# Performance work log

Hardware: AMD Instinct MI355X
Metric: run time of the kernel (lower is better)

Reference implementation:

```python
import jax, jax.numpy as jnp
import numpy as np

N_NODES = 100000
N_EDGES = 2000000
N_GRAPHS = 2000
IN_DIM = 7
EDGE_DIM = 4
HID = 32
N_CLASSES = 2
NEG_SLOPE = 0.2
BN_EPS = 1e-5


def setup_inputs() -> dict:
    key = jax.random.key(0)
    ks = jax.random.split(key, 16)
    x = jax.random.normal(ks[0], (N_NODES, IN_DIM), dtype=jnp.float32)
    edge_index = jax.random.randint(ks[1], (2, N_EDGES), 0, N_NODES, dtype=jnp.int64)
    batch = jnp.sort(jax.random.randint(ks[2], (N_NODES,), 0, N_GRAPHS, dtype=jnp.int64))
    edge_attr = jax.random.normal(ks[3], (N_EDGES, EDGE_DIM), dtype=jnp.float32)
    s = 0.1
    W0 = jax.random.normal(ks[4], (IN_DIM, HID), dtype=jnp.float32) * s
    W12 = jax.random.normal(ks[5], (2, HID, HID), dtype=jnp.float32) * s
    att_src = jax.random.normal(ks[6], (3, HID), dtype=jnp.float32) * s
    att_dst = jax.random.normal(ks[7], (3, HID), dtype=jnp.float32) * s
    lin_edge = jax.random.normal(ks[8], (3, EDGE_DIM, HID), dtype=jnp.float32) * s
    att_edge = jax.random.normal(ks[9], (3, HID), dtype=jnp.float32) * s
    bias = jnp.zeros((3, HID), dtype=jnp.float32)
    bn_gamma = jnp.ones((3, HID), dtype=jnp.float32)
    bn_beta = jnp.zeros((3, HID), dtype=jnp.float32)
    fc_W = jax.random.normal(ks[10], (HID, N_CLASSES), dtype=jnp.float32) * s
    fc_b = jnp.zeros((N_CLASSES,), dtype=jnp.float32)
    return dict(x=x, edge_index=edge_index, batch=batch, edge_attr=edge_attr,
                W0=W0, W12=W12, att_src=att_src, att_dst=att_dst,
                lin_edge=lin_edge, att_edge=att_edge, bias=bias,
                bn_gamma=bn_gamma, bn_beta=bn_beta, fc_W=fc_W, fc_b=fc_b)


def gat_layer(x, src, dst, edge_attr, W, a_src, a_dst, We, a_edge, b):
    # PyG GATConv, heads=1, add_self_loops=False: edge_attr conditions attention only.
    N = x.shape[0]
    h = x @ W                                   # [N, H]
    e = edge_attr @ We                          # [E, H]
    score = ((h * a_src).sum(-1)[src]
             + (h * a_dst).sum(-1)[dst]
             + (e * a_edge).sum(-1))            # [E]
    score = jax.nn.leaky_relu(score, NEG_SLOPE)
    m = jax.ops.segment_max(score, dst, num_segments=N)
    w = jnp.exp(score - m[dst])
    denom = jax.ops.segment_sum(w, dst, num_segments=N)
    alpha = w / (denom[dst] + 1e-16)            # segment softmax over incoming edges
    out = jax.ops.segment_sum(h[src] * alpha[:, None], dst, num_segments=N)
    return out + b


def batchnorm(x, gamma, beta):
    mu = x.mean(axis=0)
    var = ((x - mu) ** 2).mean(axis=0)          # biased var, as torch BN normalization
    return (x - mu) * jax.lax.rsqrt(var + BN_EPS) * gamma + beta


def reference(x, edge_index, batch, edge_attr, W0, W12, att_src, att_dst,
              lin_edge, att_edge, bias, bn_gamma, bn_beta, fc_W, fc_b):
    src, dst = edge_index[0], edge_index[1]
    Ws = [W0, W12[0], W12[1]]
    h = x
    for l in range(3):
        h = gat_layer(h, src, dst, edge_attr, Ws[l], att_src[l], att_dst[l],
                      lin_edge[l], att_edge[l], bias[l])
        h = batchnorm(h, bn_gamma[l], bn_beta[l])
        h = jax.nn.relu(h)
    node_embs = h
    graph_emb = jax.ops.segment_sum(node_embs, batch, num_segments=N_GRAPHS)
    out = graph_emb @ fc_W + fc_b
    return (out, node_embs, graph_emb)
```

## Files before the change

### kernel.cpp

```cpp
#include <hip/hip_runtime.h>
#include <hip/hip_bf16.h>
#include <math.h>

#define N_NODES   100000
#define N_EDGES   2000000
#define N_GRAPHS  2000
#define IN_DIM    7
#define EDGE_DIM  4
#define HID       32
#define N_CLASSES 2
#define NEG_SLOPE 0.2f
#define BN_EPS    1e-5f
#define SCAN_B    1024

__device__ __forceinline__ unsigned bfbits(float f) {
    unsigned u = __float_as_uint(f);
    return (u + 0x7FFFu + ((u >> 16) & 1u)) >> 16;
}

__global__ void k_ce_all(const float* __restrict__ lin_edge, const float* __restrict__ att_edge,
                         float* __restrict__ ce3, float* __restrict__ gsum3,
                         float* __restrict__ gsq3) {
    int t = threadIdx.x;
    if (t < 12) {
        int l = t >> 2, d = t & 3;
        float s = 0.f;
        for (int k = 0; k < HID; ++k)
            s += lin_edge[(size_t)l * EDGE_DIM * HID + d * HID + k] * att_edge[l * HID + k];
        ce3[t] = s;
    }
    if (t < 3 * HID) { gsum3[t] = 0.f; gsq3[t] = 0.f; }
}

__global__ void k_hist(const int* __restrict__ dst, int* __restrict__ deg) {
    int e = blockIdx.x * blockDim.x + threadIdx.x;
    if (e < N_EDGES) atomicAdd(deg + dst[e], 1);
}

__global__ void k_scan1(const int* __restrict__ deg, int* __restrict__ offs,
                        int* __restrict__ bsum) {
    __shared__ int wsum[16];
    int t = threadIdx.x, lane = t & 63, w = t >> 6;
    int i = blockIdx.x * SCAN_B + t;
    int v = (i < N_NODES) ? deg[i] : 0;
    int x = v;
#pragma unroll
    for (int o = 1; o < 64; o <<= 1) { int y = __shfl_up(x, o, 64); if (lane >= o) x += y; }
    if (lane == 63) wsum[w] = x;
    __syncthreads();
    if (t < 16) {
        int s = wsum[t];
#pragma unroll
        for (int o = 1; o < 16; o <<= 1) { int y = __shfl_up(s, o, 16); if (t >= o) s += y; }
        wsum[t] = s;
    }
    __syncthreads();
    int excl = (w ? wsum[w - 1] : 0) + x - v;
    if (i < N_NODES) offs[i] = excl;
    if (t == 0) bsum[blockIdx.x] = wsum[15];
}

__global__ void k_scan2(int* __restrict__ bsum, int nb) {
    __shared__ int w0;
    int t = threadIdx.x, lane = t & 63, w = t >> 6;
    int v = (t < nb) ? bsum[t] : 0;
    int x = v;
#pragma unroll
    for (int o = 1; o < 64; o <<= 1) { int y = __shfl_up(x, o, 64); if (lane >= o) x += y; }
    if (w == 0 && lane == 63) w0 = x;
    __syncthreads();
    int excl = x - v + (w ? w0 : 0);
    if (t < nb) bsum[t] = excl;
}

__global__ void k_scan3(int* __restrict__ offs, const int* __restrict__ bsum,
                        int* __restrict__ cursor) {
    int i = blockIdx.x * SCAN_B + threadIdx.x;
    if (i < N_NODES) {
        int o = offs[i] + bsum[blockIdx.x];
        offs[i] = o;
        cursor[i] = o;
    }
}

__global__ void k_scatter(const int* __restrict__ src, const int* __restrict__ dst,
                          const float4* __restrict__ eattr, const float* __restrict__ ce3,
                          int* __restrict__ cursor, int4* __restrict__ pack) {
    int e = blockIdx.x * blockDim.x + threadIdx.x;
    if (e >= N_EDGES) return;
    float4 ea = eattr[e];
    float e0 = ea.x * ce3[0] + ea.y * ce3[1] + ea.z * ce3[2] + ea.w * ce3[3];
    float e1 = ea.x * ce3[4] + ea.y * ce3[5] + ea.z * ce3[6] + ea.w * ce3[7];
    float e2 = ea.x * ce3[8] + ea.y * ce3[9] + ea.z * ce3[10] + ea.w * ce3[11];
    int d = dst[e];
    int pos = atomicAdd(cursor + d, 1);
    pack[pos] = make_int4(src[e], d,
                          (int)(bfbits(e0) | (bfbits(e1) << 16)),
                          (int)bfbits(e2));
}

template <int INDIM, bool BN>
__global__ void k_linear(const float* __restrict__ in, const float* __restrict__ W,
                         const float* __restrict__ a_src, const float* __restrict__ a_dst,
                         const float* __restrict__ gsum, const float* __restrict__ gsq,
                         const float* __restrict__ gamma, const float* __restrict__ beta,
                         __hip_bfloat16* __restrict__ h, float* __restrict__ asrc,
                         float* __restrict__ adst) {
    __shared__ float Ws[INDIM * HID];
    for (int i = threadIdx.x; i < INDIM * HID; i += blockDim.x) Ws[i] = W[i];
    __syncthreads();
    int g = threadIdx.x >> 5, k = threadIdx.x & 31;
    int n = blockIdx.x * 8 + g;
    if (n >= N_NODES) return;
    float xv;
    if (BN) {
        const float invN = 1.f / (float)N_NODES;
        float mu = gsum[k] * invN;
        float var = gsq[k] * invN - mu * mu;
        var = fmaxf(var, 0.f);
        float scl = rsqrtf(var + BN_EPS) * gamma[k];
        float v = (in[(size_t)n * INDIM + k] - mu) * scl + beta[k];
        xv = fmaxf(v, 0.f);
    } else {
        xv = (k < INDIM) ? in[(size_t)n * INDIM + k] : 0.f;
    }
    float acc = 0.f;
#pragma unroll
    for (int d = 0; d < INDIM; ++d) acc += __shfl(xv, d, 32) * Ws[d * HID + k];
    h[(size_t)n * HID + k] = __float2bfloat16(acc);
    float vs = acc * a_src[k];
    float vd = acc * a_dst[k];
#pragma unroll
    for (int m = 16; m > 0; m >>= 1) {
        vs += __shfl_xor(vs, m, 32);
        vd += __shfl_xor(vd, m, 32);
    }
    if (k == 0) { asrc[n] = vs; adst[n] = vd; }
}

template <int L>
__global__ void k_edgew(const int4* __restrict__ pack, const float* __restrict__ asrc,
                        const float* __restrict__ adst, int2* __restrict__ rec) {
    int e = blockIdx.x * blockDim.x + threadIdx.x;
    if (e >= N_EDGES) return;
    int4 pk = pack[e];
    unsigned z = (unsigned)pk.z;
    float edot;
    if (L == 0)      edot = __uint_as_float((z & 0xFFFFu) << 16);
    else if (L == 1) edot = __uint_as_float(z & 0xFFFF0000u);
    else             edot = __uint_as_float(((unsigned)pk.w & 0xFFFFu) << 16);
    float sc = asrc[pk.x] + adst[pk.y] + edot;
    sc = fmaxf(sc, NEG_SLOPE * sc);
    float w = __expf(sc);
    rec[e] = make_int2(pk.x, __float_as_int(w));
}

__global__ void k_aggr(const int2* __restrict__ rec, const int* __restrict__ offs,
                       const int* __restrict__ endp, const __hip_bfloat16* __restrict__ hb,
                       const float* __restrict__ bias, float* __restrict__ out,
                       float* __restrict__ gsum, float* __restrict__ gsq) {
    __shared__ float ssum[HID], ssq[HID];
    if (threadIdx.x < HID) { ssum[threadIdx.x] = 0.f; ssq[threadIdx.x] = 0.f; }
    __syncthreads();
    int g = threadIdx.x >> 5;
    int lane = threadIdx.x & 31;
    int sub = lane >> 4;
    int c2 = lane & 15;
    int n = blockIdx.x * 8 + g;
    if (n < N_NODES) {
        int pbeg = offs[n], en = endp[n];
        float den = 0.f, a0 = 0.f, a1 = 0.f;
        for (int p = pbeg; p < en; p += 16) {
            int2 rc[8];
            unsigned hw[8];
#pragma unroll
            for (int m = 0; m < 8; ++m) {
                int q = p + 2 * m + sub;
                q = q < en ? q : en - 1;
                rc[m] = rec[q];
            }
#pragma unroll
            for (int m = 0; m < 8; ++m)
                hw[m] = *(const unsigned*)(hb + (size_t)rc[m].x * HID + 2 * c2);
#pragma unroll
            for (int m = 0; m < 8; ++m) {
                float w = (p + 2 * m + sub < en) ? __int_as_float(rc[m].y) : 0.f;
                den += w;
                float lo = __uint_as_float((hw[m] & 0xFFFFu) << 16);
                float hi = __uint_as_float(hw[m] & 0xFFFF0000u);
                a0 = fmaf(w, lo, a0);
                a1 = fmaf(w, hi, a1);
            }
        }
        den += __shfl_xor(den, 16, 32);
        a0  += __shfl_xor(a0, 16, 32);
        a1  += __shfl_xor(a1, 16, 32);
        if (sub == 0) {
            float inv = 1.f / (den + 1e-16f);
            float v0 = a0 * inv + bias[2 * c2];
            float v1 = a1 * inv + bias[2 * c2 + 1];
            *(float2*)(out + (size_t)n * HID + 2 * c2) = make_float2(v0, v1);
            atomicAdd(&ssum[2 * c2], v0);
            atomicAdd(&ssum[2 * c2 + 1], v1);
            atomicAdd(&ssq[2 * c2], v0 * v0);
            atomicAdd(&ssq[2 * c2 + 1], v1 * v1);
        }
    }
    __syncthreads();
    if (threadIdx.x < HID) {
        atomicAdd(gsum + threadIdx.x, ssum[threadIdx.x]);
        atomicAdd(gsq + threadIdx.x, ssq[threadIdx.x]);
    }
}

__global__ void k_bn_relu_pool(const float* __restrict__ acc, const float* __restrict__ gsum,
                               const float* __restrict__ gsq, const float* __restrict__ gamma,
                               const float* __restrict__ beta, const int* __restrict__ batch,
                               float* __restrict__ nemb, float* __restrict__ gemb) {
    int g = threadIdx.x >> 5, k = threadIdx.x & 31;
    int n = blockIdx.x * 8 + g;
    if (n >= N_NODES) return;
    const float invN = 1.f / (float)N_NODES;
    float mu = gsum[k] * invN;
    float var = gsq[k] * invN - mu * mu;
    var = fmaxf(var, 0.f);
    float scl = rsqrtf(var + BN_EPS) * gamma[k];
    float v = (acc[(size_t)n * HID + k] - mu) * scl + beta[k];
    v = fmaxf(v, 0.f);
    nemb[(size_t)n * HID + k] = v;
    atomicAdd(gemb + (size_t)batch[n] * HID + k, v);
}

__global__ void k_fc(const float* __restrict__ gemb, const float* __restrict__ W,
                     const float* __restrict__ b, float* __restrict__ out) {
    int g = blockIdx.x * blockDim.x + threadIdx.x;
    if (g >= N_GRAPHS) return;
    float a0 = b[0], a1 = b[1];
    for (int k = 0; k < HID; ++k) {
        float v = gemb[(size_t)g * HID + k];
        a0 += v * W[k * 2 + 0];
        a1 += v * W[k * 2 + 1];
    }
    out[g * 2 + 0] = a0;
    out[g * 2 + 1] = a1;
}

extern "C" void kernel_launch(void* const* d_in, const int* in_sizes, int n_in,
                              void* d_out, int out_size, void* d_ws, size_t ws_size,
                              hipStream_t stream) {
    const float* x        = (const float*)d_in[0];
    const int*   ei       = (const int*)d_in[1];
    const int*   batch    = (const int*)d_in[2];
    const float* eattr    = (const float*)d_in[3];
    const float* W0       = (const float*)d_in[4];
    const float* W12      = (const float*)d_in[5];
    const float* att_src  = (const float*)d_in[6];
    const float* att_dst  = (const float*)d_in[7];
    const float* lin_edge = (const float*)d_in[8];
    const float* att_edge = (const float*)d_in[9];
    const float* bias     = (const float*)d_in[10];
    const float* bn_gamma = (const float*)d_in[11];
    const float* bn_beta  = (const float*)d_in[12];
    const float* fc_W     = (const float*)d_in[13];
    const float* fc_b     = (const float*)d_in[14];

    const int* srcA = ei;
    const int* dstA = ei + N_EDGES;

    float* out       = (float*)d_out;
    float* node_embs = out + N_GRAPHS * N_CLASSES;
    float* graph_emb = node_embs + (size_t)N_NODES * HID;

    char* ws = (char*)d_ws;
    size_t off = 0;
    auto alloc = [&](size_t bytes) { char* p = ws + off; off += (bytes + 255) & ~(size_t)255; return p; };
    __hip_bfloat16* hT = (__hip_bfloat16*)alloc((size_t)N_NODES * HID * 2);
    float* A     = (float*)alloc((size_t)N_NODES * HID * 4);
    int4*  pack  = (int4*)alloc((size_t)N_EDGES * 16);
    int2*  rec   = (int2*)alloc((size_t)N_EDGES * 8);
    int*   deg   = (int*)alloc((size_t)N_NODES * 4);
    int*   offs  = (int*)alloc((size_t)N_NODES * 4);
    int*   cursor= (int*)alloc((size_t)N_NODES * 4);
    int*   bsum  = (int*)alloc(128 * 4);
    float* asrc  = (float*)alloc((size_t)N_NODES * 4);
    float* adst  = (float*)alloc((size_t)N_NODES * 4);
    float* ce3   = (float*)alloc(12 * 4);
    float* gsum3 = (float*)alloc(3 * HID * 4);
    float* gsq3  = (float*)alloc(3 * HID * 4);
    (void)ws_size;

    const int nodeBlocks8 = (N_NODES + 7) / 8;
    const int edgeBlocks  = (N_EDGES + 255) / 256;
    const int scanBlocks  = (N_NODES + SCAN_B - 1) / SCAN_B;

    hipMemsetAsync(deg, 0, (size_t)N_NODES * 4, stream);
    k_ce_all<<<1, 128, 0, stream>>>(lin_edge, att_edge, ce3, gsum3, gsq3);
    k_hist<<<edgeBlocks, 256, 0, stream>>>(dstA, deg);
    k_scan1<<<scanBlocks, SCAN_B, 0, stream>>>(deg, offs, bsum);
    k_scan2<<<1, 128, 0, stream>>>(bsum, scanBlocks);
    k_scan3<<<scanBlocks, SCAN_B, 0, stream>>>(offs, bsum, cursor);
    k_scatter<<<edgeBlocks, 256, 0, stream>>>(srcA, dstA, (const float4*)eattr, ce3, cursor, pack);

    k_linear<IN_DIM, false><<<nodeBlocks8, 256, 0, stream>>>(
        x, W0, att_src, att_dst, nullptr, nullptr, nullptr, nullptr, hT, asrc, adst);
    k_edgew<0><<<edgeBlocks, 256, 0, stream>>>(pack, asrc, adst, rec);
    k_aggr<<<nodeBlocks8, 256, 0, stream>>>(rec, offs, cursor, hT, bias, A, gsum3, gsq3);
    k_linear<HID, true><<<nodeBlocks8, 256, 0, stream>>>(
        A, W12, att_src + HID, att_dst + HID, gsum3, gsq3, bn_gamma, bn_beta, hT, asrc, adst);
    k_edgew<1><<<edgeBlocks, 256, 0, stream>>>(pack, asrc, adst, rec);
    k_aggr<<<nodeBlocks8, 256, 0, stream>>>(rec, offs, cursor, hT, bias + HID, A,
                                            gsum3 + HID, gsq3 + HID);
    k_linear<HID, true><<<nodeBlocks8, 256, 0, stream>>>(
        A, W12 + HID * HID, att_src + 2 * HID, att_dst + 2 * HID,
        gsum3 + HID, gsq3 + HID, bn_gamma + HID, bn_beta + HID, hT, asrc, adst);
    k_edgew<2><<<edgeBlocks, 256, 0, stream>>>(pack, asrc, adst, rec);
    k_aggr<<<nodeBlocks8, 256, 0, stream>>>(rec, offs, cursor, hT, bias + 2 * HID, A,
                                            gsum3 + 2 * HID, gsq3 + 2 * HID);

    hipMemsetAsync(graph_emb, 0, (size_t)N_GRAPHS * HID * 4, stream);
    k_bn_relu_pool<<<nodeBlocks8, 256, 0, stream>>>(A, gsum3 + 2 * HID, gsq3 + 2 * HID,
                                                    bn_gamma + 2 * HID, bn_beta + 2 * HID,
                                                    batch, node_embs, graph_emb);
    k_fc<<<(N_GRAPHS + 255) / 256, 256, 0, stream>>>(graph_emb, fc_W, fc_b, out);
}
```

Baseline: 963.4 us.

## Fuse edge-weight computation into CSR aggregation kernel

Removes the separate per-layer edge-weight kernel that read the 16-byte packed edge record, gathered asrc/adst, and wrote an 8-byte (src, weight) record. The aggregation kernel now reads the packed record directly, gathers asrc per edge, uses the node's own adst once, and computes leaky-relu and exp inline. This drops three kernel launches and the write and reread of the intermediate record array. The cost is that aggregation reads 16 bytes per edge instead of 8 and does redundant exp/gather work across the 16 lanes sharing each edge.

```diff
diff --git a/kernel.cpp b/kernel.cpp
--- a/kernel.cpp
+++ b/kernel.cpp
@@ -94,9 +94,9 @@
     float e2 = ea.x * ce3[8] + ea.y * ce3[9] + ea.z * ce3[10] + ea.w * ce3[11];
     int d = dst[e];
     int pos = atomicAdd(cursor + d, 1);
-    pack[pos] = make_int4(src[e], d,
+    pack[pos] = make_int4(src[e],
                           (int)(bfbits(e0) | (bfbits(e1) << 16)),
-                          (int)bfbits(e2));
+                          (int)bfbits(e2), 0);
 }
 
 template <int INDIM, bool BN>
@@ -139,24 +139,9 @@
 }
 
 template <int L>
-__global__ void k_edgew(const int4* __restrict__ pack, const float* __restrict__ asrc,
-                        const float* __restrict__ adst, int2* __restrict__ rec) {
-    int e = blockIdx.x * blockDim.x + threadIdx.x;
-    if (e >= N_EDGES) return;
-    int4 pk = pack[e];
-    unsigned z = (unsigned)pk.z;
-    float edot;
-    if (L == 0)      edot = __uint_as_float((z & 0xFFFFu) << 16);
-    else if (L == 1) edot = __uint_as_float(z & 0xFFFF0000u);
-    else             edot = __uint_as_float(((unsigned)pk.w & 0xFFFFu) << 16);
-    float sc = asrc[pk.x] + adst[pk.y] + edot;
-    sc = fmaxf(sc, NEG_SLOPE * sc);
-    float w = __expf(sc);
-    rec[e] = make_int2(pk.x, __float_as_int(w));
-}
-
-__global__ void k_aggr(const int2* __restrict__ rec, const int* __restrict__ offs,
+__global__ void k_aggr(const int4* __restrict__ pack, const int* __restrict__ offs,
                        const int* __restrict__ endp, const __hip_bfloat16* __restrict__ hb,
+                       const float* __restrict__ asrc, const float* __restrict__ adst,
                        const float* __restrict__ bias, float* __restrict__ out,
                        float* __restrict__ gsum, float* __restrict__ gsq) {
     __shared__ float ssum[HID], ssq[HID];
@@ -169,22 +154,33 @@
     int n = blockIdx.x * 8 + g;
     if (n < N_NODES) {
         int pbeg = offs[n], en = endp[n];
+        float ad = adst[n];
         float den = 0.f, a0 = 0.f, a1 = 0.f;
         for (int p = pbeg; p < en; p += 16) {
-            int2 rc[8];
+            int4 pk[8];
+            float as[8];
             unsigned hw[8];
 #pragma unroll
             for (int m = 0; m < 8; ++m) {
                 int q = p + 2 * m + sub;
                 q = q < en ? q : en - 1;
-                rc[m] = rec[q];
+                pk[m] = pack[q];
             }
 #pragma unroll
+            for (int m = 0; m < 8; ++m) as[m] = asrc[pk[m].x];
+#pragma unroll
             for (int m = 0; m < 8; ++m)
-                hw[m] = *(const unsigned*)(hb + (size_t)rc[m].x * HID + 2 * c2);
+                hw[m] = *(const unsigned*)(hb + (size_t)pk[m].x * HID + 2 * c2);
 #pragma unroll
             for (int m = 0; m < 8; ++m) {
-                float w = (p + 2 * m + sub < en) ? __int_as_float(rc[m].y) : 0.f;
+                unsigned z = (unsigned)pk[m].y;
+                float edot;
+                if (L == 0)      edot = __uint_as_float((z & 0xFFFFu) << 16);
+                else if (L == 1) edot = __uint_as_float(z & 0xFFFF0000u);
+                else             edot = __uint_as_float(((unsigned)pk[m].z & 0xFFFFu) << 16);
+                float sc = as[m] + ad + edot;
+                sc = fmaxf(sc, NEG_SLOPE * sc);
+                float w = (p + 2 * m + sub < en) ? __expf(sc) : 0.f;
                 den += w;
                 float lo = __uint_as_float((hw[m] & 0xFFFFu) << 16);
                 float hi = __uint_as_float(hw[m] & 0xFFFF0000u);
@@ -277,7 +273,6 @@
     __hip_bfloat16* hT = (__hip_bfloat16*)alloc((size_t)N_NODES * HID * 2);
     float* A     = (float*)alloc((size_t)N_NODES * HID * 4);
     int4*  pack  = (int4*)alloc((size_t)N_EDGES * 16);
-    int2*  rec   = (int2*)alloc((size_t)N_EDGES * 8);
     int*   deg   = (int*)alloc((size_t)N_NODES * 4);
     int*   offs  = (int*)alloc((size_t)N_NODES * 4);
     int*   cursor= (int*)alloc((size_t)N_NODES * 4);
@@ -303,19 +298,17 @@
 
     k_linear<IN_DIM, false><<<nodeBlocks8, 256, 0, stream>>>(
         x, W0, att_src, att_dst, nullptr, nullptr, nullptr, nullptr, hT, asrc, adst);
-    k_edgew<0><<<edgeBlocks, 256, 0, stream>>>(pack, asrc, adst, rec);
-    k_aggr<<<nodeBlocks8, 256, 0, stream>>>(rec, offs, cursor, hT, bias, A, gsum3, gsq3);
+    k_aggr<0><<<nodeBlocks8, 256, 0, stream>>>(pack, offs, cursor, hT, asrc, adst,
+                                               bias, A, gsum3, gsq3);
     k_linear<HID, true><<<nodeBlocks8, 256, 0, stream>>>(
         A, W12, att_src + HID, att_dst + HID, gsum3, gsq3, bn_gamma, bn_beta, hT, asrc, adst);
-    k_edgew<1><<<edgeBlocks, 256, 0, stream>>>(pack, asrc, adst, rec);
-    k_aggr<<<nodeBlocks8, 256, 0, stream>>>(rec, offs, cursor, hT, bias + HID, A,
-                                            gsum3 + HID, gsq3 + HID);
+    k_aggr<1><<<nodeBlocks8, 256, 0, stream>>>(pack, offs, cursor, hT, asrc, adst,
+                                               bias + HID, A, gsum3 + HID, gsq3 + HID);
     k_linear<HID, true><<<nodeBlocks8, 256, 0, stream>>>(
         A, W12 + HID * HID, att_src + 2 * HID, att_dst + 2 * HID,
         gsum3 + HID, gsq3 + HID, bn_gamma + HID, bn_beta + HID, hT, asrc, adst);
-    k_edgew<2><<<edgeBlocks, 256, 0, stream>>>(pack, asrc, adst, rec);
-    k_aggr<<<nodeBlocks8, 256, 0, stream>>>(rec, offs, cursor, hT, bias + 2 * HID, A,
-                                            gsum3 + 2 * HID, gsq3 + 2 * HID);
+    k_aggr<2><<<nodeBlocks8, 256, 0, stream>>>(pack, offs, cursor, hT, asrc, adst,
+                                               bias + 2 * HID, A, gsum3 + 2 * HID, gsq3 + 2 * HID);
 
     hipMemsetAsync(graph_emb, 0, (size_t)N_GRAPHS * HID * 4, stream);
     k_bn_relu_pool<<<nodeBlocks8, 256, 0, stream>>>(A, gsum3 + 2 * HID, gsq3 + 2 * HID,
```

Measured after the change: 930.4 us. 1.04x faster.
